# Performance work log

Hardware: AMD Instinct MI355X
Metric: run time of the kernel (lower is better)

The kernel has to match this reference:

```python
import jax, jax.numpy as jnp
import numpy as np

N = 100000
E = 1600000
D_IN = 64
D_OUT = 64

def setup_inputs() -> dict:
    key = jax.random.key(0)
    k1, k2, k3 = jax.random.split(key, 3)
    x = jax.random.normal(k1, (N, D_IN), dtype=jnp.float32)
    edge_index = jax.random.randint(k2, (2, E), 0, N, dtype=jnp.int32)
    W = jax.random.normal(k3, (D_IN, D_OUT), dtype=jnp.float32) * (1.0 / np.sqrt(D_IN))
    b = jnp.zeros((D_OUT,), dtype=jnp.float32)
    return {"x": x, "edge_index": edge_index, "W": W, "b": b}

def reference(x, edge_index, W, b):
    # GCN.forward in eval mode: dropout is identity; GCNConv with
    # normalize=True, add_self_loops=True, edge_weight=None (all ones).
    loop = jnp.arange(N, dtype=edge_index.dtype)
    row = jnp.concatenate([edge_index[0], loop])   # source nodes, [E+N]
    col = jnp.concatenate([edge_index[1], loop])   # target nodes, [E+N]
    ew = jnp.ones(row.shape[0], dtype=x.dtype)
    # symmetric normalization: deg over targets, norm = d^-1/2[row] * d^-1/2[col]
    deg = jax.ops.segment_sum(ew, col, num_segments=N)
    dinv = jnp.where(deg > 0, jax.lax.rsqrt(deg), 0.0)
    norm = dinv[row] * dinv[col]                   # [E+N]
    h = x @ W                                      # [N, D_OUT] dense GEMM first (PyG order)
    msg = h[row] * norm[:, None]                   # gather + scale, [E+N, D_OUT]
    out = jax.ops.segment_sum(msg, col, num_segments=N)  # scatter-add aggregate
    return out + b
```

## Files before the change

kernel.cpp:

```cpp
#include <hip/hip_runtime.h>
#include <hip/hip_fp16.h>
#include <math.h>

constexpr int D = 64;
constexpr int BNODES = 128;
constexpr int BSHIFT = 7;
constexpr int BSTRIDE = 3072;
constexpr int PCHUNK = 4096;
constexpr int NB_MAX = 1024;

typedef _Float16 half8 __attribute__((ext_vector_type(8)));
typedef float floatx4 __attribute__((ext_vector_type(4)));

__global__ __launch_bounds__(256) void k_init(const float* __restrict__ W,
                                              __half* __restrict__ Wt,
                                              int* __restrict__ bcur, int NB) {
    const int i = blockIdx.x * 256 + threadIdx.x;
    if (i < NB) bcur[i] = i * BSTRIDE;
    if (i < D * D) {
        const int j = i >> 6;
        const int k = i & 63;
        Wt[i] = __float2half(W[k * D + j]);
    }
}

__global__ __launch_bounds__(512) void k_partition(
        const int* __restrict__ ei, int* __restrict__ bcur,
        unsigned* __restrict__ ebuf, int E, int NB) {
    __shared__ int lh[NB_MAX];
    __shared__ int lb[NB_MAX];
    const int t = threadIdx.x;
    for (int j = t; j < NB; j += 512) lh[j] = 0;
    __syncthreads();
    const int e0 = blockIdx.x * PCHUNK;
    const int e1 = min(e0 + PCHUNK, E);
    for (int e = e0 + t; e < e1; e += 512)
        atomicAdd(&lh[ei[E + e] >> BSHIFT], 1);
    __syncthreads();
    for (int j = t; j < NB; j += 512) {
        const int n = lh[j];
        lb[j] = n ? atomicAdd(&bcur[j], n) : 0;
        lh[j] = 0;
    }
    __syncthreads();
    for (int e = e0 + t; e < e1; e += 512) {
        const int r = ei[e];
        const int c = ei[E + e];
        const int bkt = c >> BSHIFT;
        const int rank = atomicAdd(&lh[bkt], 1);
        const int pos = lb[bkt] + rank;
        if (pos < (bkt + 1) * BSTRIDE)
            ebuf[pos] = ((unsigned)r << BSHIFT) | (unsigned)(c & (BNODES - 1));
    }
}

__global__ __launch_bounds__(256) void k_cnt(
        const unsigned* __restrict__ ebuf, const int* __restrict__ bcur,
        int* __restrict__ cnt, int N) {
    __shared__ int lh[BNODES];
    const int j = blockIdx.x;
    const int t = threadIdx.x;
    const int s0 = j * BSTRIDE;
    const int s1 = min(bcur[j], s0 + BSTRIDE);
    if (t < BNODES) lh[t] = 0;
    __syncthreads();
    for (int i = s0 + t; i < s1; i += 256)
        atomicAdd(&lh[ebuf[i] & (BNODES - 1)], 1);
    __syncthreads();
    const int node = (j << BSHIFT) + t;
    if (t < BNODES && node < N) cnt[node] = lh[t];
}

__global__ __launch_bounds__(256) void k_gemm_mfma(
        const float* __restrict__ x, const __half* __restrict__ Wt,
        const int* __restrict__ cnt, __half* __restrict__ gh, int N) {
    const int tile = (blockIdx.x * 256 + threadIdx.x) >> 6;
    const int nt = N >> 4;
    if (tile >= nt) return;
    const int lane = threadIdx.x & 63;
    const int r16  = lane & 15;
    const int kq   = lane >> 4;

    const _Float16* wt = (const _Float16*)Wt;
    half8 bf[4][2];
#pragma unroll
    for (int jt = 0; jt < 4; ++jt)
#pragma unroll
        for (int s = 0; s < 2; ++s)
            bf[jt][s] = *(const half8*)(wt + (jt * 16 + r16) * D + s * 32 + kq * 8);

    half8 af[2];
#pragma unroll
    for (int s = 0; s < 2; ++s) {
        const float4* xp = reinterpret_cast<const float4*>(
            x + (size_t)(tile * 16 + r16) * D + s * 32 + kq * 8);
        const float4 x0 = xp[0];
        const float4 x1 = xp[1];
        half8 a;
        a[0] = (_Float16)x0.x; a[1] = (_Float16)x0.y;
        a[2] = (_Float16)x0.z; a[3] = (_Float16)x0.w;
        a[4] = (_Float16)x1.x; a[5] = (_Float16)x1.y;
        a[6] = (_Float16)x1.z; a[7] = (_Float16)x1.w;
        af[s] = a;
    }

    floatx4 acc[4];
#pragma unroll
    for (int jt = 0; jt < 4; ++jt) {
        acc[jt] = (floatx4){0.f, 0.f, 0.f, 0.f};
        acc[jt] = __builtin_amdgcn_mfma_f32_16x16x32_f16(af[0], bf[jt][0], acc[jt], 0, 0, 0);
        acc[jt] = __builtin_amdgcn_mfma_f32_16x16x32_f16(af[1], bf[jt][1], acc[jt], 0, 0, 0);
    }

#pragma unroll
    for (int r = 0; r < 4; ++r) {
        const int node = tile * 16 + kq * 4 + r;
        const float dinv = rsqrtf((float)(cnt[node] + 1));
#pragma unroll
        for (int jt = 0; jt < 4; ++jt)
            gh[(size_t)node * D + jt * 16 + r16] = __float2half(acc[jt][r] * dinv);
    }
}

__global__ __launch_bounds__(512) void k_breduce(
        const unsigned* __restrict__ ebuf, const int* __restrict__ bcur,
        const __half* __restrict__ gh, const float* __restrict__ b,
        float* __restrict__ out, int N) {
    __shared__ int srcLDS[BSTRIDE];
    __shared__ int lh[BNODES];
    __shared__ int st[BNODES];
    __shared__ int lcur[BNODES];
    const int j = blockIdx.x;
    const int t = threadIdx.x;
    const int s0 = j * BSTRIDE;
    const int s1 = min(bcur[j], s0 + BSTRIDE);
    const int base = j << BSHIFT;
    const int nn = min(BNODES, N - base);

    if (t < BNODES) lh[t] = 0;
    __syncthreads();
    for (int i = s0 + t; i < s1; i += 512)
        atomicAdd(&lh[ebuf[i] & (BNODES - 1)], 1);
    __syncthreads();
    if (t < BNODES) st[t] = lh[t];
    __syncthreads();
    for (int off = 1; off < BNODES; off <<= 1) {
        int y = 0;
        if (t < BNODES && t >= off) y = st[t - off];
        __syncthreads();
        if (t < BNODES && t >= off) st[t] += y;
        __syncthreads();
    }
    if (t < BNODES) {
        const int s = st[t] - lh[t];
        st[t] = s;
        lcur[t] = s;
    }
    __syncthreads();
    for (int i = s0 + t; i < s1; i += 512) {
        const unsigned code = ebuf[i];
        const int c = code & (BNODES - 1);
        const int rank = atomicAdd(&lcur[c], 1);
        srcLDS[rank] = (int)(code >> BSHIFT);
    }
    __syncthreads();

    const int g8 = t >> 3;
    const int fl = t & 7;

    const uint4* g4 = reinterpret_cast<const uint4*>(gh);
    const float4* b4 = reinterpret_cast<const float4*>(b);
    float4* o4 = reinterpret_cast<float4*>(out);
    const __half2 z = __float2half2_rn(0.f);
    const float4 bb0 = b4[fl * 2];
    const float4 bb1 = b4[fl * 2 + 1];

#pragma unroll
    for (int q = 0; q < 2; ++q) {
        const int nl = q * 64 + g8;
        if (nl >= nn) continue;
        const int node = base + nl;
        const int start = st[nl];
        const int num = lh[nl];

        const uint4 su = g4[(size_t)node * 8 + fl];
        __half2 a0 = *(const __half2*)&su.x;
        __half2 a1 = *(const __half2*)&su.y;
        __half2 a2 = *(const __half2*)&su.z;
        __half2 a3 = *(const __half2*)&su.w;
        __half2 c0 = z, c1 = z, c2 = z, c3 = z;

        int i = start;
        const int end = start + num;
        for (; i + 2 <= end; i += 2) {
            const int r0 = srcLDS[i];
            const int r1 = srcLDS[i + 1];
            const uint4 u0 = g4[(size_t)r0 * 8 + fl];
            const uint4 u1 = g4[(size_t)r1 * 8 + fl];
            a0 = __hadd2(a0, *(const __half2*)&u0.x);
            a1 = __hadd2(a1, *(const __half2*)&u0.y);
            a2 = __hadd2(a2, *(const __half2*)&u0.z);
            a3 = __hadd2(a3, *(const __half2*)&u0.w);
            c0 = __hadd2(c0, *(const __half2*)&u1.x);
            c1 = __hadd2(c1, *(const __half2*)&u1.y);
            c2 = __hadd2(c2, *(const __half2*)&u1.z);
            c3 = __hadd2(c3, *(const __half2*)&u1.w);
        }
        if (i < end) {
            const int r = srcLDS[i];
            const uint4 u = g4[(size_t)r * 8 + fl];
            a0 = __hadd2(a0, *(const __half2*)&u.x);
            a1 = __hadd2(a1, *(const __half2*)&u.y);
            a2 = __hadd2(a2, *(const __half2*)&u.z);
            a3 = __hadd2(a3, *(const __half2*)&u.w);
        }
        a0 = __hadd2(a0, c0);
        a1 = __hadd2(a1, c1);
        a2 = __hadd2(a2, c2);
        a3 = __hadd2(a3, c3);

        const float dinv = rsqrtf((float)(num + 1));
        const float2 f0 = __half22float2(a0);
        const float2 f1 = __half22float2(a1);
        const float2 f2 = __half22float2(a2);
        const float2 f3 = __half22float2(a3);
        float4 o0, o1;
        o0.x = fmaf(dinv, f0.x, bb0.x); o0.y = fmaf(dinv, f0.y, bb0.y);
        o0.z = fmaf(dinv, f1.x, bb0.z); o0.w = fmaf(dinv, f1.y, bb0.w);
        o1.x = fmaf(dinv, f2.x, bb1.x); o1.y = fmaf(dinv, f2.y, bb1.y);
        o1.z = fmaf(dinv, f3.x, bb1.z); o1.w = fmaf(dinv, f3.y, bb1.w);
        o4[(size_t)node * 16 + fl * 2]     = o0;
        o4[(size_t)node * 16 + fl * 2 + 1] = o1;
    }
}

extern "C" void kernel_launch(void* const* d_in, const int* in_sizes, int n_in,
                              void* d_out, int out_size, void* d_ws, size_t ws_size,
                              hipStream_t stream) {
    const float* x  = (const float*)d_in[0];
    const int*   ei = (const int*)d_in[1];
    const float* W  = (const float*)d_in[2];
    const float* b  = (const float*)d_in[3];
    float* out = (float*)d_out;

    const int N = in_sizes[0] / D;
    const int E = in_sizes[1] / 2;
    const int NB = (N + BNODES - 1) >> BSHIFT;
    const int blocksP = (E + PCHUNK - 1) / PCHUNK;

    __half*   gh   = (__half*)d_ws;
    int*      cnt  = (int*)(gh + (size_t)N * D);
    int*      bcur = cnt + N;
    __half*   Wt   = (__half*)(bcur + NB);
    unsigned* ebuf = (unsigned*)(Wt + D * D);

    k_init     <<<16, 256, 0, stream>>>(W, Wt, bcur, NB);
    k_partition<<<blocksP, 512, 0, stream>>>(ei, bcur, ebuf, E, NB);
    k_cnt      <<<NB, 256, 0, stream>>>(ebuf, bcur, cnt, N);
    k_gemm_mfma<<<((N / 16) * 64 + 255) / 256, 256, 0, stream>>>(x, Wt, cnt, gh, N);
    k_breduce  <<<NB, 512, 0, stream>>>(ebuf, bcur, gh, b, out, N);
}
```

Baseline: 85.52 us.

## Cache edge codes in LDS and sort nodes by degree for balanced reduction

```diff
diff --git a/kernel.cpp b/kernel.cpp
--- a/kernel.cpp
+++ b/kernel.cpp
@@ -29,13 +29,17 @@
         unsigned* __restrict__ ebuf, int E, int NB) {
     __shared__ int lh[NB_MAX];
     __shared__ int lb[NB_MAX];
+    __shared__ int cc[PCHUNK];
     const int t = threadIdx.x;
     for (int j = t; j < NB; j += 512) lh[j] = 0;
     __syncthreads();
     const int e0 = blockIdx.x * PCHUNK;
     const int e1 = min(e0 + PCHUNK, E);
-    for (int e = e0 + t; e < e1; e += 512)
-        atomicAdd(&lh[ei[E + e] >> BSHIFT], 1);
+    for (int e = e0 + t; e < e1; e += 512) {
+        const int c = ei[E + e];
+        cc[e - e0] = c;
+        atomicAdd(&lh[c >> BSHIFT], 1);
+    }
     __syncthreads();
     for (int j = t; j < NB; j += 512) {
         const int n = lh[j];
@@ -45,7 +49,7 @@
     __syncthreads();
     for (int e = e0 + t; e < e1; e += 512) {
         const int r = ei[e];
-        const int c = ei[E + e];
+        const int c = cc[e - e0];
         const int bkt = c >> BSHIFT;
         const int rank = atomicAdd(&lh[bkt], 1);
         const int pos = lb[bkt] + rank;
@@ -54,7 +58,7 @@
     }
 }
 
-__global__ __launch_bounds__(256) void k_cnt(
+__global__ __launch_bounds__(512) void k_cnt(
         const unsigned* __restrict__ ebuf, const int* __restrict__ bcur,
         int* __restrict__ cnt, int N) {
     __shared__ int lh[BNODES];
@@ -64,7 +68,7 @@
     const int s1 = min(bcur[j], s0 + BSTRIDE);
     if (t < BNODES) lh[t] = 0;
     __syncthreads();
-    for (int i = s0 + t; i < s1; i += 256)
+    for (int i = s0 + t; i < s1; i += 512)
         atomicAdd(&lh[ebuf[i] & (BNODES - 1)], 1);
     __syncthreads();
     const int node = (j << BSHIFT) + t;
@@ -126,21 +130,26 @@
         const unsigned* __restrict__ ebuf, const int* __restrict__ bcur,
         const __half* __restrict__ gh, const float* __restrict__ b,
         float* __restrict__ out, int N) {
+    __shared__ int codes[BSTRIDE];
     __shared__ int srcLDS[BSTRIDE];
     __shared__ int lh[BNODES];
     __shared__ int st[BNODES];
     __shared__ int lcur[BNODES];
+    __shared__ int keys[BNODES];
     const int j = blockIdx.x;
     const int t = threadIdx.x;
     const int s0 = j * BSTRIDE;
-    const int s1 = min(bcur[j], s0 + BSTRIDE);
+    const int ne = min(bcur[j], s0 + BSTRIDE) - s0;
     const int base = j << BSHIFT;
     const int nn = min(BNODES, N - base);
 
     if (t < BNODES) lh[t] = 0;
     __syncthreads();
-    for (int i = s0 + t; i < s1; i += 512)
-        atomicAdd(&lh[ebuf[i] & (BNODES - 1)], 1);
+    for (int i = t; i < ne; i += 512) {
+        const int code = (int)ebuf[s0 + i];
+        codes[i] = code;
+        atomicAdd(&lh[code & (BNODES - 1)], 1);
+    }
     __syncthreads();
     if (t < BNODES) st[t] = lh[t];
     __syncthreads();
@@ -155,13 +164,27 @@
         const int s = st[t] - lh[t];
         st[t] = s;
         lcur[t] = s;
-    }
-    __syncthreads();
-    for (int i = s0 + t; i < s1; i += 512) {
-        const unsigned code = ebuf[i];
+        keys[t] = (lh[t] << BSHIFT) | t;
+    }
+    __syncthreads();
+    for (int i = t; i < ne; i += 512) {
+        const int code = codes[i];
         const int c = code & (BNODES - 1);
         const int rank = atomicAdd(&lcur[c], 1);
-        srcLDS[rank] = (int)(code >> BSHIFT);
+        srcLDS[rank] = code >> BSHIFT;
+    }
+    for (int k = 2; k <= BNODES; k <<= 1) {
+        for (int jj = k >> 1; jj > 0; jj >>= 1) {
+            __syncthreads();
+            if (t < BNODES) {
+                const int p = t ^ jj;
+                if (p > t) {
+                    const int a = keys[t], bk = keys[p];
+                    const bool asc = ((t & k) == 0);
+                    if (asc ? (a > bk) : (a < bk)) { keys[t] = bk; keys[p] = a; }
+                }
+            }
+        }
     }
     __syncthreads();
 
@@ -177,11 +200,12 @@
 
 #pragma unroll
     for (int q = 0; q < 2; ++q) {
-        const int nl = q * 64 + g8;
+        const int key = keys[q * 64 + g8];
+        const int nl = key & (BNODES - 1);
         if (nl >= nn) continue;
+        const int num = key >> BSHIFT;
         const int node = base + nl;
         const int start = st[nl];
-        const int num = lh[nl];
 
         const uint4 su = g4[(size_t)node * 8 + fl];
         __half2 a0 = *(const __half2*)&su.x;
@@ -256,7 +280,7 @@
 
     k_init     <<<16, 256, 0, stream>>>(W, Wt, bcur, NB);
     k_partition<<<blocksP, 512, 0, stream>>>(ei, bcur, ebuf, E, NB);
-    k_cnt      <<<NB, 256, 0, stream>>>(ebuf, bcur, cnt, N);
+    k_cnt      <<<NB, 512, 0, stream>>>(ebuf, bcur, cnt, N);
     k_gemm_mfma<<<((N / 16) * 64 + 255) / 256, 256, 0, stream>>>(x, Wt, cnt, gh, N);
     k_breduce  <<<NB, 512, 0, stream>>>(ebuf, bcur, gh, b, out, N);
 }
```

After: 87.32 us. 1.02x slower.

## Fuse degree count into GEMM, split features into halves, vectorize partition loads

Applied to the files above, without the earlier changes.

```diff
diff --git a/kernel.cpp b/kernel.cpp
--- a/kernel.cpp
+++ b/kernel.cpp
@@ -29,13 +29,31 @@
         unsigned* __restrict__ ebuf, int E, int NB) {
     __shared__ int lh[NB_MAX];
     __shared__ int lb[NB_MAX];
+    __shared__ int cc[PCHUNK];
     const int t = threadIdx.x;
     for (int j = t; j < NB; j += 512) lh[j] = 0;
     __syncthreads();
     const int e0 = blockIdx.x * PCHUNK;
     const int e1 = min(e0 + PCHUNK, E);
-    for (int e = e0 + t; e < e1; e += 512)
-        atomicAdd(&lh[ei[E + e] >> BSHIFT], 1);
+    const bool full = (e1 - e0 == PCHUNK);
+
+    if (full) {
+        const int4* cp = reinterpret_cast<const int4*>(ei + E + e0);
+        const int4 ca = cp[t];
+        const int4 cb = cp[t + 512];
+        reinterpret_cast<int4*>(cc)[t]       = ca;
+        reinterpret_cast<int4*>(cc)[t + 512] = cb;
+        atomicAdd(&lh[ca.x >> BSHIFT], 1); atomicAdd(&lh[ca.y >> BSHIFT], 1);
+        atomicAdd(&lh[ca.z >> BSHIFT], 1); atomicAdd(&lh[ca.w >> BSHIFT], 1);
+        atomicAdd(&lh[cb.x >> BSHIFT], 1); atomicAdd(&lh[cb.y >> BSHIFT], 1);
+        atomicAdd(&lh[cb.z >> BSHIFT], 1); atomicAdd(&lh[cb.w >> BSHIFT], 1);
+    } else {
+        for (int e = e0 + t; e < e1; e += 512) {
+            const int c = ei[E + e];
+            cc[e - e0] = c;
+            atomicAdd(&lh[c >> BSHIFT], 1);
+        }
+    }
     __syncthreads();
     for (int j = t; j < NB; j += 512) {
         const int n = lh[j];
@@ -43,41 +61,56 @@
         lh[j] = 0;
     }
     __syncthreads();
-    for (int e = e0 + t; e < e1; e += 512) {
-        const int r = ei[e];
-        const int c = ei[E + e];
-        const int bkt = c >> BSHIFT;
-        const int rank = atomicAdd(&lh[bkt], 1);
-        const int pos = lb[bkt] + rank;
-        if (pos < (bkt + 1) * BSTRIDE)
-            ebuf[pos] = ((unsigned)r << BSHIFT) | (unsigned)(c & (BNODES - 1));
-    }
-}
-
-__global__ __launch_bounds__(256) void k_cnt(
+
+    if (full) {
+        const int4* rp = reinterpret_cast<const int4*>(ei + e0);
+        const int4 ra = rp[t];
+        const int4 rb = rp[t + 512];
+        const int r8[8] = {ra.x, ra.y, ra.z, ra.w, rb.x, rb.y, rb.z, rb.w};
+#pragma unroll
+        for (int k = 0; k < 8; ++k) {
+            const int ci = (k < 4) ? (4 * t + k) : (2048 + 4 * t + (k - 4));
+            const int c = cc[ci];
+            const int bkt = c >> BSHIFT;
+            const int rank = atomicAdd(&lh[bkt], 1);
+            const int pos = lb[bkt] + rank;
+            if (pos < (bkt + 1) * BSTRIDE)
+                ebuf[pos] = ((unsigned)r8[k] << BSHIFT) | (unsigned)(c & (BNODES - 1));
+        }
+    } else {
+        for (int e = e0 + t; e < e1; e += 512) {
+            const int r = ei[e];
+            const int c = cc[e - e0];
+            const int bkt = c >> BSHIFT;
+            const int rank = atomicAdd(&lh[bkt], 1);
+            const int pos = lb[bkt] + rank;
+            if (pos < (bkt + 1) * BSTRIDE)
+                ebuf[pos] = ((unsigned)r << BSHIFT) | (unsigned)(c & (BNODES - 1));
+        }
+    }
+}
+
+__global__ __launch_bounds__(512) void k_gemm_fused(
+        const float* __restrict__ x, const __half* __restrict__ Wt,
         const unsigned* __restrict__ ebuf, const int* __restrict__ bcur,
-        int* __restrict__ cnt, int N) {
+        __half* __restrict__ gh0, __half* __restrict__ gh1, int N) {
     __shared__ int lh[BNODES];
     const int j = blockIdx.x;
     const int t = threadIdx.x;
+    const int base = j << BSHIFT;
     const int s0 = j * BSTRIDE;
     const int s1 = min(bcur[j], s0 + BSTRIDE);
+
     if (t < BNODES) lh[t] = 0;
     __syncthreads();
-    for (int i = s0 + t; i < s1; i += 256)
+    for (int i = s0 + t; i < s1; i += 512)
         atomicAdd(&lh[ebuf[i] & (BNODES - 1)], 1);
     __syncthreads();
-    const int node = (j << BSHIFT) + t;
-    if (t < BNODES && node < N) cnt[node] = lh[t];
-}
-
-__global__ __launch_bounds__(256) void k_gemm_mfma(
-        const float* __restrict__ x, const __half* __restrict__ Wt,
-        const int* __restrict__ cnt, __half* __restrict__ gh, int N) {
-    const int tile = (blockIdx.x * 256 + threadIdx.x) >> 6;
-    const int nt = N >> 4;
-    if (tile >= nt) return;
-    const int lane = threadIdx.x & 63;
+
+    const int wave = t >> 6;
+    const int node16 = base + wave * 16;
+    if (node16 >= N) return;
+    const int lane = t & 63;
     const int r16  = lane & 15;
     const int kq   = lane >> 4;
 
@@ -93,7 +126,7 @@
 #pragma unroll
     for (int s = 0; s < 2; ++s) {
         const float4* xp = reinterpret_cast<const float4*>(
-            x + (size_t)(tile * 16 + r16) * D + s * 32 + kq * 8);
+            x + (size_t)(node16 + r16) * D + s * 32 + kq * 8);
         const float4 x0 = xp[0];
         const float4 x1 = xp[1];
         half8 a;
@@ -114,18 +147,22 @@
 
 #pragma unroll
     for (int r = 0; r < 4; ++r) {
-        const int node = tile * 16 + kq * 4 + r;
-        const float dinv = rsqrtf((float)(cnt[node] + 1));
-#pragma unroll
-        for (int jt = 0; jt < 4; ++jt)
-            gh[(size_t)node * D + jt * 16 + r16] = __float2half(acc[jt][r] * dinv);
+        const int nl = wave * 16 + kq * 4 + r;
+        const int node = base + nl;
+        const float dinv = rsqrtf((float)(lh[nl] + 1));
+#pragma unroll
+        for (int jt = 0; jt < 2; ++jt)
+            gh0[(size_t)node * 32 + jt * 16 + r16] = __float2half(acc[jt][r] * dinv);
+#pragma unroll
+        for (int jt = 2; jt < 4; ++jt)
+            gh1[(size_t)node * 32 + (jt - 2) * 16 + r16] = __float2half(acc[jt][r] * dinv);
     }
 }
 
 __global__ __launch_bounds__(512) void k_breduce(
         const unsigned* __restrict__ ebuf, const int* __restrict__ bcur,
-        const __half* __restrict__ gh, const float* __restrict__ b,
-        float* __restrict__ out, int N) {
+        const __half* __restrict__ gh0, const __half* __restrict__ gh1,
+        const float* __restrict__ b, float* __restrict__ out, int N) {
     __shared__ int srcLDS[BSTRIDE];
     __shared__ int lh[BNODES];
     __shared__ int st[BNODES];
@@ -165,25 +202,23 @@
     }
     __syncthreads();
 
-    const int g8 = t >> 3;
-    const int fl = t & 7;
-
-    const uint4* g4 = reinterpret_cast<const uint4*>(gh);
+    const int g  = t >> 2;
+    const int fl = t & 3;
+    if (g >= nn) return;
+
+    const int node = base + g;
+    const int start = st[g];
+    const int num = lh[g];
+    const float dinv = rsqrtf((float)(num + 1));
     const float4* b4 = reinterpret_cast<const float4*>(b);
     float4* o4 = reinterpret_cast<float4*>(out);
     const __half2 z = __float2half2_rn(0.f);
-    const float4 bb0 = b4[fl * 2];
-    const float4 bb1 = b4[fl * 2 + 1];
-
-#pragma unroll
-    for (int q = 0; q < 2; ++q) {
-        const int nl = q * 64 + g8;
-        if (nl >= nn) continue;
-        const int node = base + nl;
-        const int start = st[nl];
-        const int num = lh[nl];
-
-        const uint4 su = g4[(size_t)node * 8 + fl];
+
+#pragma unroll
+    for (int phase = 0; phase < 2; ++phase) {
+        const uint4* gp = reinterpret_cast<const uint4*>(phase ? gh1 : gh0);
+
+        const uint4 su = gp[(size_t)node * 4 + fl];
         __half2 a0 = *(const __half2*)&su.x;
         __half2 a1 = *(const __half2*)&su.y;
         __half2 a2 = *(const __half2*)&su.z;
@@ -195,8 +230,8 @@
         for (; i + 2 <= end; i += 2) {
             const int r0 = srcLDS[i];
             const int r1 = srcLDS[i + 1];
-            const uint4 u0 = g4[(size_t)r0 * 8 + fl];
-            const uint4 u1 = g4[(size_t)r1 * 8 + fl];
+            const uint4 u0 = gp[(size_t)r0 * 4 + fl];
+            const uint4 u1 = gp[(size_t)r1 * 4 + fl];
             a0 = __hadd2(a0, *(const __half2*)&u0.x);
             a1 = __hadd2(a1, *(const __half2*)&u0.y);
             a2 = __hadd2(a2, *(const __half2*)&u0.z);
@@ -208,7 +243,7 @@
         }
         if (i < end) {
             const int r = srcLDS[i];
-            const uint4 u = g4[(size_t)r * 8 + fl];
+            const uint4 u = gp[(size_t)r * 4 + fl];
             a0 = __hadd2(a0, *(const __half2*)&u.x);
             a1 = __hadd2(a1, *(const __half2*)&u.y);
             a2 = __hadd2(a2, *(const __half2*)&u.z);
@@ -219,18 +254,20 @@
         a2 = __hadd2(a2, c2);
         a3 = __hadd2(a3, c3);
 
-        const float dinv = rsqrtf((float)(num + 1));
         const float2 f0 = __half22float2(a0);
         const float2 f1 = __half22float2(a1);
         const float2 f2 = __half22float2(a2);
         const float2 f3 = __half22float2(a3);
+        const int ob = phase * 8 + fl * 2;
+        const float4 bb0 = b4[ob];
+        const float4 bb1 = b4[ob + 1];
         float4 o0, o1;
         o0.x = fmaf(dinv, f0.x, bb0.x); o0.y = fmaf(dinv, f0.y, bb0.y);
         o0.z = fmaf(dinv, f1.x, bb0.z); o0.w = fmaf(dinv, f1.y, bb0.w);
         o1.x = fmaf(dinv, f2.x, bb1.x); o1.y = fmaf(dinv, f2.y, bb1.y);
         o1.z = fmaf(dinv, f3.x, bb1.z); o1.w = fmaf(dinv, f3.y, bb1.w);
-        o4[(size_t)node * 16 + fl * 2]     = o0;
-        o4[(size_t)node * 16 + fl * 2 + 1] = o1;
+        o4[(size_t)node * 16 + ob]     = o0;
+        o4[(size_t)node * 16 + ob + 1] = o1;
     }
 }
 
@@ -248,15 +285,14 @@
     const int NB = (N + BNODES - 1) >> BSHIFT;
     const int blocksP = (E + PCHUNK - 1) / PCHUNK;
 
-    __half*   gh   = (__half*)d_ws;
-    int*      cnt  = (int*)(gh + (size_t)N * D);
-    int*      bcur = cnt + N;
-    __half*   Wt   = (__half*)(bcur + NB);
+    __half*   gh0  = (__half*)d_ws;
+    __half*   gh1  = gh0 + (size_t)N * 32;
+    __half*   Wt   = gh1 + (size_t)N * 32;
     unsigned* ebuf = (unsigned*)(Wt + D * D);
-
-    k_init     <<<16, 256, 0, stream>>>(W, Wt, bcur, NB);
-    k_partition<<<blocksP, 512, 0, stream>>>(ei, bcur, ebuf, E, NB);
-    k_cnt      <<<NB, 256, 0, stream>>>(ebuf, bcur, cnt, N);
-    k_gemm_mfma<<<((N / 16) * 64 + 255) / 256, 256, 0, stream>>>(x, Wt, cnt, gh, N);
-    k_breduce  <<<NB, 512, 0, stream>>>(ebuf, bcur, gh, b, out, N);
-}
+    int*      bcur = (int*)(ebuf + (size_t)NB * BSTRIDE);
+
+    k_init      <<<16, 256, 0, stream>>>(W, Wt, bcur, NB);
+    k_partition <<<blocksP, 512, 0, stream>>>(ei, bcur, ebuf, E, NB);
+    k_gemm_fused<<<NB, 512, 0, stream>>>(x, Wt, ebuf, bcur, gh0, gh1, N);
+    k_breduce   <<<NB, 512, 0, stream>>>(ebuf, bcur, gh0, gh1, b, out, N);
+}
```

New measurement: 88.98 us, median of 2. +4.0%, slower.
